# Performance work log

Measured on AMD Instinct MI355X. Metric: run time of the kernel, lower is better.

The kernel has to match this reference:

```python
import jax, jax.numpy as jnp
import numpy as np

B, T, C, H = 8, 2048, 1024, 64


def setup_inputs() -> dict:
    key = jax.random.key(0)
    k1, k2, k3, k4 = jax.random.split(key, 4)
    data = jax.random.normal(k1, (B, T, C), dtype=jnp.float32)
    # nn.Linear(embed, head, bias=False) weights, stored as [embed, head] so y = x @ W
    scale = C ** -0.5  # init-scale so activations stay O(1)
    Wq = jax.random.normal(k2, (C, H), dtype=jnp.float32) * scale
    Wk = jax.random.normal(k3, (C, H), dtype=jnp.float32) * scale
    Wv = jax.random.normal(k4, (C, H), dtype=jnp.float32) * scale
    return {"data": data, "Wq": Wq, "Wk": Wk, "Wv": Wv}


def reference(data, Wq, Wk, Wv):
    # data: [B, T, C]; self-attention (crossData=None), causal mask, eval-mode dropout.
    Bs, Ts, Cs = data.shape
    q = data @ Wq  # [B, T, H]
    k = data @ Wk  # [B, T, H]
    v = data @ Wv  # [B, T, H]
    # NOTE: original scales by C**-0.5 with C = embed_size (faithful to source).
    wei = jnp.einsum('btd,bsd->bts', q, k) * (Cs ** -0.5)  # [B, T, T]
    causal = jnp.tril(jnp.ones((Ts, Ts), dtype=bool))
    wei = jnp.where(causal[None, :, :], wei, -jnp.inf)
    wei = jax.nn.softmax(wei, axis=-1)
    out = jnp.einsum('bts,bsh->bth', wei, v)  # [B, T, H]
    return out
```

## Files before the change

kernel.cpp:

```cpp
#include <hip/hip_runtime.h>
#include <hip/hip_bf16.h>


typedef __bf16 bf16;
typedef __bf16 bf16x8 __attribute__((ext_vector_type(8)));
typedef float f32x4 __attribute__((ext_vector_type(4)));
typedef unsigned int u32;
typedef u32 u32x2 __attribute__((ext_vector_type(2)));
typedef u32 u32x4 __attribute__((ext_vector_type(4)));

#define T_SZ 2048
#define C_SZ 1024
#define H_SZ 64
#define QOFF 0
#define KOFF 1024
#define VOFF 2048
#define PPITCH 72
#define NEG_BIG (-30000.0f)
#define QSCALE 0.04508422f

__device__ __forceinline__ bf16x8 ld8(const bf16* p) { return *(const bf16x8*)p; }

template <int CTRL>
__device__ __forceinline__ float dpp_mov(float x) {
  return __builtin_bit_cast(float,
      __builtin_amdgcn_update_dpp(0, __builtin_bit_cast(int, x), CTRL, 0xf, 0xf, true));
}
__device__ __forceinline__ float qmax16(float x) {
  x = fmaxf(x, dpp_mov<0x121>(x));
  x = fmaxf(x, dpp_mov<0x122>(x));
  x = fmaxf(x, dpp_mov<0x124>(x));
  x = fmaxf(x, dpp_mov<0x128>(x));
  return x;
}
__device__ __forceinline__ float qsum16(float x) {
  x += dpp_mov<0x121>(x);
  x += dpp_mov<0x122>(x);
  x += dpp_mov<0x124>(x);
  x += dpp_mov<0x128>(x);
  return x;
}

__global__ __launch_bounds__(256) void transpose_w(const float* __restrict__ Wq,
                                                   const float* __restrict__ Wk,
                                                   const float* __restrict__ Wv,
                                                   bf16* __restrict__ Wp) {
  __shared__ float sh[64][65];
  int ct = blockIdx.x;
  int mat = blockIdx.y;
  const float* W = (mat == 0) ? Wq : (mat == 1 ? Wk : Wv);
  int tid = threadIdx.x;
  int r = tid >> 2, cb = (tid & 3) * 16;

  const f32x4* src = (const f32x4*)(W + (size_t)(ct * 64 + r) * H_SZ + cb);
#pragma unroll
  for (int v = 0; v < 4; ++v) {
    f32x4 x = src[v];
#pragma unroll
    for (int jx = 0; jx < 4; ++jx) sh[r][cb + v * 4 + jx] = x[jx];
  }
  __syncthreads();

  float scale = (mat == 0) ? QSCALE : 1.0f;
  bf16x8 o0, o1;
#pragma unroll
  for (int jx = 0; jx < 8; ++jx) o0[jx] = (bf16)(sh[cb + jx][r] * scale);
#pragma unroll
  for (int jx = 0; jx < 8; ++jx) o1[jx] = (bf16)(sh[cb + 8 + jx][r] * scale);

  int jj = mat * 4 + (r >> 4);
  int l15 = r & 15;
  int c0 = ct * 64 + cb;
  int kci = c0 >> 5;
  int qa = (c0 >> 3) & 3;
  bf16* dst = Wp + (size_t)(jj * 32 + kci) * 512 + l15 * 32 + qa * 8;
  *(bf16x8*)dst = o0;
  *(bf16x8*)(dst + 8) = o1;
}

__global__ __launch_bounds__(768, 3) void qkv(const float* data, const bf16* __restrict__ Wp,
                                              bf16* arena, int regsz) {
  __shared__ bf16 As[64 * 1024];
  char* As_b = (char*)As;
  int blk = blockIdx.x;
  int tid = threadIdx.x;
  int w = tid >> 6, lane = tid & 63;
  int l15 = lane & 15, quad = lane >> 4;

  const float* src = data + (size_t)blk * 64 * C_SZ;
#pragma unroll
  for (int g = 0; g < 3; ++g) {
    f32x4 st[7];
#pragma unroll
    for (int i = 0; i < 7; ++i) {
      int u = (g * 7 + i) * 768 + tid;
      st[i] = __builtin_nontemporal_load(
          (const f32x4*)(src + (size_t)(u >> 8) * C_SZ + (u & 255) * 4));
    }
#pragma unroll
    for (int i = 0; i < 7; ++i) {
      int u = (g * 7 + i) * 768 + tid;
      int row = u >> 8, c4 = u & 255;
      bf16 t4[4] = {(bf16)st[i][0], (bf16)st[i][1], (bf16)st[i][2], (bf16)st[i][3]};
      int bo = ((c4 >> 3) << 12) + row * 64 + (c4 & 7) * 8;
      *(u32x2*)(As_b + bo) = *(const u32x2*)t4;
    }
  }
  if (tid < 256) {
    int c4 = tid;
    f32x4 x = __builtin_nontemporal_load(
        (const f32x4*)(src + (size_t)63 * C_SZ + c4 * 4));
    bf16 t4[4] = {(bf16)x[0], (bf16)x[1], (bf16)x[2], (bf16)x[3]};
    int bo = ((c4 >> 3) << 12) + 63 * 64 + (c4 & 7) * 8;
    *(u32x2*)(As_b + bo) = *(const u32x2*)t4;
  }
  __syncthreads();

  int j = w;
  const bf16* wb = Wp + (size_t)j * 32 * 512 + l15 * 32 + quad * 8;
  bf16x8 wf[2];
  wf[0] = ld8(wb);
  wf[1] = ld8(wb + 512);

  f32x4 acc[4];
  f32x4 zero = {0.f, 0.f, 0.f, 0.f};
#pragma unroll
  for (int rg = 0; rg < 4; ++rg) acc[rg] = zero;

  bool isQK = (j < 8);
  int lbase = l15 * 64 + quad * 16;

#pragma unroll 2
  for (int kci = 0; kci < 32; ++kci) {
    int cur = kci & 1;
    bf16x8 df[4];
#pragma unroll
    for (int rg = 0; rg < 4; ++rg) {
      int bo = (kci << 12) + rg * 1024 + lbase;
      df[rg] = ld8((const bf16*)(As_b + bo));
    }
    if (isQK) {
#pragma unroll
      for (int rg = 0; rg < 4; ++rg)
        acc[rg] = __builtin_amdgcn_mfma_f32_16x16x32_bf16(wf[cur], df[rg], acc[rg], 0, 0, 0);
    } else {
#pragma unroll
      for (int rg = 0; rg < 4; ++rg)
        acc[rg] = __builtin_amdgcn_mfma_f32_16x16x32_bf16(df[rg], wf[cur], acc[rg], 0, 0, 0);
    }
    wf[cur] = ld8(wb + ((kci + 2) & 31) * 512);
  }

#pragma unroll
  for (int rg = 0; rg < 4; ++rg) {
    bf16* reg = arena + (size_t)(blk * 4 + rg) * (size_t)regsz;
    bf16 p4[4] = {(bf16)acc[rg][0], (bf16)acc[rg][1], (bf16)acc[rg][2], (bf16)acc[rg][3]};
    if (j < 4) {
      bf16* dst = reg + QOFF + l15 * 64 + j * 16 + quad * 4;
      *(u32x2*)dst = *(const u32x2*)p4;
    } else if (j < 8) {
      int jk = j - 4;
      bf16* dst = reg + KOFF + (jk >> 1) * 512 + l15 * 32 + (jk & 1) * 16 + quad * 4;
      *(u32x2*)dst = *(const u32x2*)p4;
    } else {
      bf16* dst = reg + VOFF + ((j - 8) * 16 + l15) * 16 + quad * 4;
      *(u32x2*)dst = *(const u32x2*)p4;
    }
  }
}

__global__ __launch_bounds__(256, 4) void attn(const bf16* __restrict__ arena,
                                               float* __restrict__ out, int regsz) {
  __shared__ bf16 Ps[4][16 * PPITCH];
  __shared__ f32x4 Mg[3][6][64];
  int id = blockIdx.x;
  int b = id & 7;
  int t = id >> 3;
  int slice = t & 3;
  int qt = 31 - (t >> 2);
  int tid = threadIdx.x;
  int w = tid >> 6, lane = tid & 63;
  int l15 = lane & 15, quad = lane >> 4;

  const bf16* base = arena + (size_t)b * 128 * (size_t)regsz;

  const bf16* qreg = base + (size_t)(qt * 4 + slice) * (size_t)regsz + QOFF + l15 * 64;
  bf16x8 qf0 = ld8(qreg + quad * 8);
  bf16x8 qf1 = ld8(qreg + 32 + quad * 8);

  f32x4 accO[4];
  f32x4 zero = {0.f, 0.f, 0.f, 0.f};
#pragma unroll
  for (int nt = 0; nt < 4; ++nt) accO[nt] = zero;
  float m[4], l[4];
#pragma unroll
  for (int r = 0; r < 4; ++r) { m[r] = NEG_BIG; l[r] = 0.f; }

  int qrow_base = qt * 64 + slice * 16 + quad * 4;
  int vro = (quad >> 1);
  int vco = (quad & 1) * 8;

  int q4 = (qt + 4) >> 2;
  int kbeg = w * q4;
  int kend = min((w + 1) * q4, qt + 1);

  for (int kt = kbeg; kt < kend; ++kt) {
    bf16x8 kf[8];
#pragma unroll
    for (int nt = 0; nt < 4; ++nt) {
      const bf16* kp = base + (size_t)(kt * 4 + nt) * (size_t)regsz + KOFF + l15 * 32 + quad * 8;
      kf[2 * nt] = ld8(kp);
      kf[2 * nt + 1] = ld8(kp + 512);
    }

    f32x4 sA[4];
#pragma unroll
    for (int nt = 0; nt < 4; ++nt) sA[nt] = zero;
#pragma unroll
    for (int nt = 0; nt < 4; ++nt) {
      sA[nt] = __builtin_amdgcn_mfma_f32_16x16x32_bf16(qf0, kf[2 * nt], sA[nt], 0, 0, 0);
      sA[nt] = __builtin_amdgcn_mfma_f32_16x16x32_bf16(qf1, kf[2 * nt + 1], sA[nt], 0, 0, 0);
    }

    bf16x8 vf0[4];
#pragma unroll
    for (int nt = 0; nt < 4; ++nt) {
      const bf16* vp = base + (size_t)(kt * 4 + vro) * (size_t)regsz + VOFF +
                       (nt * 16 + l15) * 16 + vco;
      vf0[nt] = ld8(vp);
    }

    if (kt == qt) {
#pragma unroll
      for (int nt = 0; nt < 4; ++nt) {
        int colg = kt * 64 + nt * 16 + l15;
#pragma unroll
        for (int r = 0; r < 4; ++r)
          if (colg > qrow_base + r) sA[nt][r] = NEG_BIG;
      }
    }

    float alpha[4];
#pragma unroll
    for (int r = 0; r < 4; ++r) {
      float mx = qmax16(fmaxf(fmaxf(sA[0][r], sA[1][r]), fmaxf(sA[2][r], sA[3][r])));
      float mnew = fmaxf(m[r], mx);
      alpha[r] = exp2f(m[r] - mnew);
      m[r] = mnew;
    }

    float rs[4] = {0.f, 0.f, 0.f, 0.f};
#pragma unroll
    for (int nt = 0; nt < 4; ++nt) {
#pragma unroll
      for (int r = 0; r < 4; ++r) {
        float p = exp2f(sA[nt][r] - m[r]);
        sA[nt][r] = p;
        rs[r] += p;
      }
    }
#pragma unroll
    for (int r = 0; r < 4; ++r) l[r] = l[r] * alpha[r] + qsum16(rs[r]);

#pragma unroll
    for (int nt = 0; nt < 4; ++nt) {
#pragma unroll
      for (int r = 0; r < 4; ++r)
        Ps[w][(quad * 4 + r) * PPITCH + nt * 16 + l15] = (bf16)sA[nt][r];
    }

    bf16x8 vf1[4];
#pragma unroll
    for (int nt = 0; nt < 4; ++nt) {
      const bf16* vp = base + (size_t)(kt * 4 + 2 + vro) * (size_t)regsz + VOFF +
                       (nt * 16 + l15) * 16 + vco;
      vf1[nt] = ld8(vp);
    }

#pragma unroll
    for (int nt = 0; nt < 4; ++nt) {
#pragma unroll
      for (int r = 0; r < 4; ++r) accO[nt][r] *= alpha[r];
    }
    bf16x8 pf0 = ld8((const bf16*)Ps[w] + l15 * PPITCH + quad * 8);
    bf16x8 pf1 = ld8((const bf16*)Ps[w] + l15 * PPITCH + 32 + quad * 8);
#pragma unroll
    for (int nt = 0; nt < 4; ++nt)
      accO[nt] = __builtin_amdgcn_mfma_f32_16x16x32_bf16(pf0, vf0[nt], accO[nt], 0, 0, 0);
#pragma unroll
    for (int nt = 0; nt < 4; ++nt)
      accO[nt] = __builtin_amdgcn_mfma_f32_16x16x32_bf16(pf1, vf1[nt], accO[nt], 0, 0, 0);
  }

  if (w > 0) {
#pragma unroll
    for (int nt = 0; nt < 4; ++nt) Mg[w - 1][nt][lane] = accO[nt];
    f32x4 mv = {m[0], m[1], m[2], m[3]};
    f32x4 lv = {l[0], l[1], l[2], l[3]};
    Mg[w - 1][4][lane] = mv;
    Mg[w - 1][5][lane] = lv;
  }
  __syncthreads();
  if (w == 0) {
#pragma unroll
    for (int wv = 0; wv < 3; ++wv) {
      f32x4 mo = Mg[wv][4][lane];
      f32x4 lo = Mg[wv][5][lane];
      f32x4 oo[4];
#pragma unroll
      for (int nt = 0; nt < 4; ++nt) oo[nt] = Mg[wv][nt][lane];
#pragma unroll
      for (int r = 0; r < 4; ++r) {
        float mnew = fmaxf(m[r], mo[r]);
        float a = exp2f(m[r] - mnew);
        float bs = exp2f(mo[r] - mnew);
        l[r] = l[r] * a + lo[r] * bs;
#pragma unroll
        for (int nt = 0; nt < 4; ++nt) accO[nt][r] = accO[nt][r] * a + oo[nt][r] * bs;
        m[r] = mnew;
      }
    }

    float inv[4];
#pragma unroll
    for (int r = 0; r < 4; ++r) inv[r] = 1.f / l[r];
#pragma unroll
    for (int nt = 0; nt < 4; ++nt) {
#pragma unroll
      for (int r = 0; r < 4; ++r) {
        int tk = qt * 64 + slice * 16 + quad * 4 + r;
        int h = nt * 16 + l15;
        out[((size_t)b * T_SZ + tk) * H_SZ + h] = accO[nt][r] * inv[r];
      }
    }
  }
}

extern "C" void kernel_launch(void* const* d_in, const int* in_sizes, int n_in,
                              void* d_out, int out_size, void* d_ws, size_t ws_size,
                              hipStream_t stream) {
  const float* data = (const float*)d_in[0];

  const size_t arena_bytes = (size_t)1024 * 4096 * sizeof(bf16);
  const size_t wt_bytes = (size_t)3 * H_SZ * C_SZ * sizeof(bf16);
  bool ws_ok = (d_ws != nullptr) && (ws_size >= arena_bytes + wt_bytes);

  bf16* arena = ws_ok ? (bf16*)d_ws : (bf16*)d_in[0];
  bf16* Wp = ws_ok ? (bf16*)((char*)d_ws + arena_bytes) : (bf16*)d_out;
  int regsz = ws_ok ? 4096 : 32768;

  transpose_w<<<dim3(16, 3), 256, 0, stream>>>((const float*)d_in[1],
                                               (const float*)d_in[2],
                                               (const float*)d_in[3], Wp);
  qkv<<<256, 768, 0, stream>>>(data, Wp, arena, regsz);
  attn<<<1024, 256, 0, stream>>>(arena, (float*)d_out, regsz);
}
```

Before: 130.0 us.

## Double-buffer QKV projection input staging to overlap global loads with MFMA

The qkv kernel used to load and convert the full 64x1024 fp32 input tile into a 128KB LDS buffer before any MFMA work. It now stages the K dimension in four 256-column chunks across two 32KB LDS buffers, issuing global loads for the next chunk before computing on the current one. This is meant to hide global load latency behind matrix math and to cut LDS use, which could raise occupancy. The cost is a block-wide barrier per chunk and more live registers for the prefetched data.

Measured after the change: 131.6 us. Within noise of the previous version (+1.2%).

```diff
diff --git a/kernel.cpp b/kernel.cpp
--- a/kernel.cpp
+++ b/kernel.cpp
@@ -80,7 +80,7 @@
 
 __global__ __launch_bounds__(768, 3) void qkv(const float* data, const bf16* __restrict__ Wp,
                                               bf16* arena, int regsz) {
-  __shared__ bf16 As[64 * 1024];
+  __shared__ bf16 As[2 * 16384];
   char* As_b = (char*)As;
   int blk = blockIdx.x;
   int tid = threadIdx.x;
@@ -88,31 +88,26 @@
   int l15 = lane & 15, quad = lane >> 4;
 
   const float* src = data + (size_t)blk * 64 * C_SZ;
-#pragma unroll
-  for (int g = 0; g < 3; ++g) {
-    f32x4 st[7];
-#pragma unroll
-    for (int i = 0; i < 7; ++i) {
-      int u = (g * 7 + i) * 768 + tid;
+
+  f32x4 st[6];
+#pragma unroll
+  for (int i = 0; i < 6; ++i) {
+    if (i < 5 || tid < 256) {
+      int v = i * 768 + tid;
+      int row = v >> 6, c4l = v & 63;
       st[i] = __builtin_nontemporal_load(
-          (const f32x4*)(src + (size_t)(u >> 8) * C_SZ + (u & 255) * 4));
-    }
-#pragma unroll
-    for (int i = 0; i < 7; ++i) {
-      int u = (g * 7 + i) * 768 + tid;
-      int row = u >> 8, c4 = u & 255;
+          (const f32x4*)(src + (size_t)row * C_SZ + c4l * 4));
+    }
+  }
+#pragma unroll
+  for (int i = 0; i < 6; ++i) {
+    if (i < 5 || tid < 256) {
+      int v = i * 768 + tid;
+      int row = v >> 6, c4l = v & 63;
       bf16 t4[4] = {(bf16)st[i][0], (bf16)st[i][1], (bf16)st[i][2], (bf16)st[i][3]};
-      int bo = ((c4 >> 3) << 12) + row * 64 + (c4 & 7) * 8;
+      int bo = ((c4l >> 3) << 12) + row * 64 + (c4l & 7) * 8;
       *(u32x2*)(As_b + bo) = *(const u32x2*)t4;
     }
-  }
-  if (tid < 256) {
-    int c4 = tid;
-    f32x4 x = __builtin_nontemporal_load(
-        (const f32x4*)(src + (size_t)63 * C_SZ + c4 * 4));
-    bf16 t4[4] = {(bf16)x[0], (bf16)x[1], (bf16)x[2], (bf16)x[3]};
-    int bo = ((c4 >> 3) << 12) + 63 * 64 + (c4 & 7) * 8;
-    *(u32x2*)(As_b + bo) = *(const u32x2*)t4;
   }
   __syncthreads();
 
@@ -130,25 +125,56 @@
   bool isQK = (j < 8);
   int lbase = l15 * 64 + quad * 16;
 
-#pragma unroll 2
-  for (int kci = 0; kci < 32; ++kci) {
-    int cur = kci & 1;
-    bf16x8 df[4];
-#pragma unroll
-    for (int rg = 0; rg < 4; ++rg) {
-      int bo = (kci << 12) + rg * 1024 + lbase;
-      df[rg] = ld8((const bf16*)(As_b + bo));
-    }
-    if (isQK) {
+#pragma unroll
+  for (int c = 0; c < 4; ++c) {
+    if (c < 3) {
+#pragma unroll
+      for (int i = 0; i < 6; ++i) {
+        if (i < 5 || tid < 256) {
+          int v = i * 768 + tid;
+          int row = v >> 6, c4l = v & 63;
+          st[i] = __builtin_nontemporal_load(
+              (const f32x4*)(src + (size_t)row * C_SZ + ((c + 1) * 64 + c4l) * 4));
+        }
+      }
+      __builtin_amdgcn_sched_barrier(0);
+    }
+
+    int rb = (c & 1) * 32768;
+#pragma unroll
+    for (int kl = 0; kl < 8; ++kl) {
+      int kci = c * 8 + kl;
+      int cur = kci & 1;
+      bf16x8 df[4];
 #pragma unroll
       for (int rg = 0; rg < 4; ++rg)
-        acc[rg] = __builtin_amdgcn_mfma_f32_16x16x32_bf16(wf[cur], df[rg], acc[rg], 0, 0, 0);
-    } else {
-#pragma unroll
-      for (int rg = 0; rg < 4; ++rg)
-        acc[rg] = __builtin_amdgcn_mfma_f32_16x16x32_bf16(df[rg], wf[cur], acc[rg], 0, 0, 0);
-    }
-    wf[cur] = ld8(wb + ((kci + 2) & 31) * 512);
+        df[rg] = ld8((const bf16*)(As_b + rb + (kl << 12) + rg * 1024 + lbase));
+      if (isQK) {
+#pragma unroll
+        for (int rg = 0; rg < 4; ++rg)
+          acc[rg] = __builtin_amdgcn_mfma_f32_16x16x32_bf16(wf[cur], df[rg], acc[rg], 0, 0, 0);
+      } else {
+#pragma unroll
+        for (int rg = 0; rg < 4; ++rg)
+          acc[rg] = __builtin_amdgcn_mfma_f32_16x16x32_bf16(df[rg], wf[cur], acc[rg], 0, 0, 0);
+      }
+      wf[cur] = ld8(wb + ((kci + 2) & 31) * 512);
+    }
+
+    if (c < 3) {
+      int wbuf = ((c + 1) & 1) * 32768;
+#pragma unroll
+      for (int i = 0; i < 6; ++i) {
+        if (i < 5 || tid < 256) {
+          int v = i * 768 + tid;
+          int row = v >> 6, c4l = v & 63;
+          bf16 t4[4] = {(bf16)st[i][0], (bf16)st[i][1], (bf16)st[i][2], (bf16)st[i][3]};
+          int bo = wbuf + ((c4l >> 3) << 12) + row * 64 + (c4l & 7) * 8;
+          *(u32x2*)(As_b + bo) = *(const u32x2*)t4;
+        }
+      }
+    }
+    __syncthreads();
   }
 
 #pragma unroll
```

## Split QKV projection into 32-row blocks with two output tiles per wave

Applied to the files above, without the earlier changes.

The QKV projection kernel now handles 32 rows per block instead of 64, using 384 threads and launching 512 blocks instead of 256. Each wave computes two 16-column weight tiles over two row groups, instead of one weight tile over four row groups. The goal is more blocks, filling more of the GPU's compute units, and a smaller LDS footprint for better occupancy. In exchange, each weight fragment is reused across fewer rows, so weights are loaded from global memory twice as often in total.

Result: slower. 134.9 us (+3.8%).

```diff
diff --git a/kernel.cpp b/kernel.cpp
--- a/kernel.cpp
+++ b/kernel.cpp
@@ -78,93 +78,106 @@
   *(bf16x8*)(dst + 8) = o1;
 }
 
-__global__ __launch_bounds__(768, 3) void qkv(const float* data, const bf16* __restrict__ Wp,
+__global__ __launch_bounds__(384, 3) void qkv(const float* data, const bf16* __restrict__ Wp,
                                               bf16* arena, int regsz) {
-  __shared__ bf16 As[64 * 1024];
+  __shared__ bf16 As[32 * 1024];
   char* As_b = (char*)As;
   int blk = blockIdx.x;
   int tid = threadIdx.x;
   int w = tid >> 6, lane = tid & 63;
   int l15 = lane & 15, quad = lane >> 4;
 
-  const float* src = data + (size_t)blk * 64 * C_SZ;
+  const float* src = data + (size_t)blk * 32 * C_SZ;
 #pragma unroll
   for (int g = 0; g < 3; ++g) {
     f32x4 st[7];
 #pragma unroll
     for (int i = 0; i < 7; ++i) {
-      int u = (g * 7 + i) * 768 + tid;
+      int u = (g * 7 + i) * 384 + tid;
       st[i] = __builtin_nontemporal_load(
           (const f32x4*)(src + (size_t)(u >> 8) * C_SZ + (u & 255) * 4));
     }
 #pragma unroll
     for (int i = 0; i < 7; ++i) {
-      int u = (g * 7 + i) * 768 + tid;
+      int u = (g * 7 + i) * 384 + tid;
       int row = u >> 8, c4 = u & 255;
       bf16 t4[4] = {(bf16)st[i][0], (bf16)st[i][1], (bf16)st[i][2], (bf16)st[i][3]};
-      int bo = ((c4 >> 3) << 12) + row * 64 + (c4 & 7) * 8;
+      int bo = ((c4 >> 3) << 11) + row * 64 + (c4 & 7) * 8;
       *(u32x2*)(As_b + bo) = *(const u32x2*)t4;
     }
   }
-  if (tid < 256) {
-    int c4 = tid;
+  if (tid < 128) {
+    int u = 8064 + tid;
+    int row = u >> 8, c4 = u & 255;
     f32x4 x = __builtin_nontemporal_load(
-        (const f32x4*)(src + (size_t)63 * C_SZ + c4 * 4));
+        (const f32x4*)(src + (size_t)row * C_SZ + c4 * 4));
     bf16 t4[4] = {(bf16)x[0], (bf16)x[1], (bf16)x[2], (bf16)x[3]};
-    int bo = ((c4 >> 3) << 12) + 63 * 64 + (c4 & 7) * 8;
+    int bo = ((c4 >> 3) << 11) + row * 64 + (c4 & 7) * 8;
     *(u32x2*)(As_b + bo) = *(const u32x2*)t4;
   }
   __syncthreads();
 
-  int j = w;
-  const bf16* wb = Wp + (size_t)j * 32 * 512 + l15 * 32 + quad * 8;
-  bf16x8 wf[2];
-  wf[0] = ld8(wb);
-  wf[1] = ld8(wb + 512);
-
-  f32x4 acc[4];
+  int j0 = 2 * w;
+  const bf16* wb0 = Wp + (size_t)j0 * 32 * 512 + l15 * 32 + quad * 8;
+  const bf16* wb1 = wb0 + 32 * 512;
+  bf16x8 wf0[2], wf1[2];
+  wf0[0] = ld8(wb0);
+  wf0[1] = ld8(wb0 + 512);
+  wf1[0] = ld8(wb1);
+  wf1[1] = ld8(wb1 + 512);
+
+  f32x4 acc[2][2];
   f32x4 zero = {0.f, 0.f, 0.f, 0.f};
 #pragma unroll
-  for (int rg = 0; rg < 4; ++rg) acc[rg] = zero;
-
-  bool isQK = (j < 8);
+  for (int jc = 0; jc < 2; ++jc)
+#pragma unroll
+    for (int rg = 0; rg < 2; ++rg) acc[jc][rg] = zero;
+
+  bool isQK = (j0 < 8);
   int lbase = l15 * 64 + quad * 16;
 
 #pragma unroll 2
   for (int kci = 0; kci < 32; ++kci) {
     int cur = kci & 1;
-    bf16x8 df[4];
-#pragma unroll
-    for (int rg = 0; rg < 4; ++rg) {
-      int bo = (kci << 12) + rg * 1024 + lbase;
-      df[rg] = ld8((const bf16*)(As_b + bo));
-    }
+    bf16x8 df[2];
+#pragma unroll
+    for (int rg = 0; rg < 2; ++rg)
+      df[rg] = ld8((const bf16*)(As_b + (kci << 11) + rg * 1024 + lbase));
     if (isQK) {
-#pragma unroll
-      for (int rg = 0; rg < 4; ++rg)
-        acc[rg] = __builtin_amdgcn_mfma_f32_16x16x32_bf16(wf[cur], df[rg], acc[rg], 0, 0, 0);
+      acc[0][0] = __builtin_amdgcn_mfma_f32_16x16x32_bf16(wf0[cur], df[0], acc[0][0], 0, 0, 0);
+      acc[0][1] = __builtin_amdgcn_mfma_f32_16x16x32_bf16(wf0[cur], df[1], acc[0][1], 0, 0, 0);
+      acc[1][0] = __builtin_amdgcn_mfma_f32_16x16x32_bf16(wf1[cur], df[0], acc[1][0], 0, 0, 0);
+      acc[1][1] = __builtin_amdgcn_mfma_f32_16x16x32_bf16(wf1[cur], df[1], acc[1][1], 0, 0, 0);
     } else {
-#pragma unroll
-      for (int rg = 0; rg < 4; ++rg)
-        acc[rg] = __builtin_amdgcn_mfma_f32_16x16x32_bf16(df[rg], wf[cur], acc[rg], 0, 0, 0);
-    }
-    wf[cur] = ld8(wb + ((kci + 2) & 31) * 512);
-  }
-
-#pragma unroll
-  for (int rg = 0; rg < 4; ++rg) {
-    bf16* reg = arena + (size_t)(blk * 4 + rg) * (size_t)regsz;
-    bf16 p4[4] = {(bf16)acc[rg][0], (bf16)acc[rg][1], (bf16)acc[rg][2], (bf16)acc[rg][3]};
-    if (j < 4) {
-      bf16* dst = reg + QOFF + l15 * 64 + j * 16 + quad * 4;
-      *(u32x2*)dst = *(const u32x2*)p4;
-    } else if (j < 8) {
-      int jk = j - 4;
-      bf16* dst = reg + KOFF + (jk >> 1) * 512 + l15 * 32 + (jk & 1) * 16 + quad * 4;
-      *(u32x2*)dst = *(const u32x2*)p4;
-    } else {
-      bf16* dst = reg + VOFF + ((j - 8) * 16 + l15) * 16 + quad * 4;
-      *(u32x2*)dst = *(const u32x2*)p4;
+      acc[0][0] = __builtin_amdgcn_mfma_f32_16x16x32_bf16(df[0], wf0[cur], acc[0][0], 0, 0, 0);
+      acc[0][1] = __builtin_amdgcn_mfma_f32_16x16x32_bf16(df[1], wf0[cur], acc[0][1], 0, 0, 0);
+      acc[1][0] = __builtin_amdgcn_mfma_f32_16x16x32_bf16(df[0], wf1[cur], acc[1][0], 0, 0, 0);
+      acc[1][1] = __builtin_amdgcn_mfma_f32_16x16x32_bf16(df[1], wf1[cur], acc[1][1], 0, 0, 0);
+    }
+    int knx = ((kci + 2) & 31) * 512;
+    wf0[cur] = ld8(wb0 + knx);
+    wf1[cur] = ld8(wb1 + knx);
+  }
+
+#pragma unroll
+  for (int jc = 0; jc < 2; ++jc) {
+    int j = j0 + jc;
+#pragma unroll
+    for (int rg = 0; rg < 2; ++rg) {
+      bf16* reg = arena + (size_t)(blk * 2 + rg) * (size_t)regsz;
+      bf16 p4[4] = {(bf16)acc[jc][rg][0], (bf16)acc[jc][rg][1],
+                    (bf16)acc[jc][rg][2], (bf16)acc[jc][rg][3]};
+      if (j < 4) {
+        bf16* dst = reg + QOFF + l15 * 64 + j * 16 + quad * 4;
+        *(u32x2*)dst = *(const u32x2*)p4;
+      } else if (j < 8) {
+        int jk = j - 4;
+        bf16* dst = reg + KOFF + (jk >> 1) * 512 + l15 * 32 + (jk & 1) * 16 + quad * 4;
+        *(u32x2*)dst = *(const u32x2*)p4;
+      } else {
+        bf16* dst = reg + VOFF + ((j - 8) * 16 + l15) * 16 + quad * 4;
+        *(u32x2*)dst = *(const u32x2*)p4;
+      }
     }
   }
 }
@@ -352,6 +365,6 @@
   transpose_w<<<dim3(16, 3), 256, 0, stream>>>((const float*)d_in[1],
                                                (const float*)d_in[2],
                                                (const float*)d_in[3], Wp);
-  qkv<<<256, 768, 0, stream>>>(data, Wp, arena, regsz);
+  qkv<<<512, 384, 0, stream>>>(data, Wp, arena, regsz);
   attn<<<1024, 256, 0, stream>>>(arena, (float*)d_out, regsz);
 }
```

## Process two 16-row query slices per block and prefetch next K tile

Applied to the files above, without the earlier changes.

Each attention block now handles two 16-row query slices (32 rows) instead of one. The same K and V fragments serve both slices, which halves global K/V loads per query row, and the grid drops from 1024 to 512 blocks. The next K tile is loaded into registers before the current softmax work, and block order now pairs long and short causal rows. In exchange, register pressure roughly doubles (launch bounds lowered from 4 to 2 blocks per CU), occupancy and latency hiding drop, and the shared P buffer is reused serially for both slices.

New measurement: 132.4 us. No clear change (+1.9%).

```diff
diff --git a/kernel.cpp b/kernel.cpp
--- a/kernel.cpp
+++ b/kernel.cpp
@@ -169,34 +169,35 @@
   }
 }
 
-__global__ __launch_bounds__(256, 4) void attn(const bf16* __restrict__ arena,
+__global__ __launch_bounds__(256, 2) void attn(const bf16* __restrict__ arena,
                                                float* __restrict__ out, int regsz) {
   __shared__ bf16 Ps[4][16 * PPITCH];
-  __shared__ f32x4 Mg[3][6][64];
+  __shared__ f32x4 Mg[3][12][64];
   int id = blockIdx.x;
   int b = id & 7;
-  int t = id >> 3;
-  int slice = t & 3;
-  int qt = 31 - (t >> 2);
+  int u = id >> 3;
+  int sp = u & 1;
+  int qt = (u < 32) ? (31 - (u >> 1)) : ((u - 32) >> 1);
   int tid = threadIdx.x;
   int w = tid >> 6, lane = tid & 63;
   int l15 = lane & 15, quad = lane >> 4;
 
   const bf16* base = arena + (size_t)b * 128 * (size_t)regsz;
 
-  const bf16* qreg = base + (size_t)(qt * 4 + slice) * (size_t)regsz + QOFF + l15 * 64;
-  bf16x8 qf0 = ld8(qreg + quad * 8);
-  bf16x8 qf1 = ld8(qreg + 32 + quad * 8);
-
-  f32x4 accO[4];
+  const bf16* qregA = base + (size_t)(qt * 4 + sp * 2) * (size_t)regsz + QOFF + l15 * 64;
+  const bf16* qregB = qregA + regsz;
+  bf16x8 qfA0 = ld8(qregA + quad * 8), qfA1 = ld8(qregA + 32 + quad * 8);
+  bf16x8 qfB0 = ld8(qregB + quad * 8), qfB1 = ld8(qregB + 32 + quad * 8);
+
+  f32x4 accA[4], accB[4];
   f32x4 zero = {0.f, 0.f, 0.f, 0.f};
 #pragma unroll
-  for (int nt = 0; nt < 4; ++nt) accO[nt] = zero;
-  float m[4], l[4];
-#pragma unroll
-  for (int r = 0; r < 4; ++r) { m[r] = NEG_BIG; l[r] = 0.f; }
-
-  int qrow_base = qt * 64 + slice * 16 + quad * 4;
+  for (int nt = 0; nt < 4; ++nt) { accA[nt] = zero; accB[nt] = zero; }
+  float mA[4], lA[4], mB[4], lB[4];
+#pragma unroll
+  for (int r = 0; r < 4; ++r) { mA[r] = NEG_BIG; lA[r] = 0.f; mB[r] = NEG_BIG; lB[r] = 0.f; }
+
+  int rowA = qt * 64 + sp * 32 + quad * 4;
   int vro = (quad >> 1);
   int vco = (quad & 1) * 8;
 
@@ -204,24 +205,15 @@
   int kbeg = w * q4;
   int kend = min((w + 1) * q4, qt + 1);
 
+  bf16x8 kf[8];
+#pragma unroll
+  for (int nt = 0; nt < 4; ++nt) {
+    const bf16* kp = base + (size_t)(kbeg * 4 + nt) * (size_t)regsz + KOFF + l15 * 32 + quad * 8;
+    kf[2 * nt] = ld8(kp);
+    kf[2 * nt + 1] = ld8(kp + 512);
+  }
+
   for (int kt = kbeg; kt < kend; ++kt) {
-    bf16x8 kf[8];
-#pragma unroll
-    for (int nt = 0; nt < 4; ++nt) {
-      const bf16* kp = base + (size_t)(kt * 4 + nt) * (size_t)regsz + KOFF + l15 * 32 + quad * 8;
-      kf[2 * nt] = ld8(kp);
-      kf[2 * nt + 1] = ld8(kp + 512);
-    }
-
-    f32x4 sA[4];
-#pragma unroll
-    for (int nt = 0; nt < 4; ++nt) sA[nt] = zero;
-#pragma unroll
-    for (int nt = 0; nt < 4; ++nt) {
-      sA[nt] = __builtin_amdgcn_mfma_f32_16x16x32_bf16(qf0, kf[2 * nt], sA[nt], 0, 0, 0);
-      sA[nt] = __builtin_amdgcn_mfma_f32_16x16x32_bf16(qf1, kf[2 * nt + 1], sA[nt], 0, 0, 0);
-    }
-
     bf16x8 vf0[4];
 #pragma unroll
     for (int nt = 0; nt < 4; ++nt) {
@@ -230,43 +222,28 @@
       vf0[nt] = ld8(vp);
     }
 
-    if (kt == qt) {
+    f32x4 sA[4], sB[4];
+#pragma unroll
+    for (int nt = 0; nt < 4; ++nt) { sA[nt] = zero; sB[nt] = zero; }
+#pragma unroll
+    for (int nt = 0; nt < 4; ++nt) {
+      sA[nt] = __builtin_amdgcn_mfma_f32_16x16x32_bf16(qfA0, kf[2 * nt], sA[nt], 0, 0, 0);
+      sA[nt] = __builtin_amdgcn_mfma_f32_16x16x32_bf16(qfA1, kf[2 * nt + 1], sA[nt], 0, 0, 0);
+    }
+#pragma unroll
+    for (int nt = 0; nt < 4; ++nt) {
+      sB[nt] = __builtin_amdgcn_mfma_f32_16x16x32_bf16(qfB0, kf[2 * nt], sB[nt], 0, 0, 0);
+      sB[nt] = __builtin_amdgcn_mfma_f32_16x16x32_bf16(qfB1, kf[2 * nt + 1], sB[nt], 0, 0, 0);
+    }
+
+    if (kt + 1 < kend) {
 #pragma unroll
       for (int nt = 0; nt < 4; ++nt) {
-        int colg = kt * 64 + nt * 16 + l15;
-#pragma unroll
-        for (int r = 0; r < 4; ++r)
-          if (colg > qrow_base + r) sA[nt][r] = NEG_BIG;
-      }
-    }
-
-    float alpha[4];
-#pragma unroll
-    for (int r = 0; r < 4; ++r) {
-      float mx = qmax16(fmaxf(fmaxf(sA[0][r], sA[1][r]), fmaxf(sA[2][r], sA[3][r])));
-      float mnew = fmaxf(m[r], mx);
-      alpha[r] = exp2f(m[r] - mnew);
-      m[r] = mnew;
-    }
-
-    float rs[4] = {0.f, 0.f, 0.f, 0.f};
-#pragma unroll
-    for (int nt = 0; nt < 4; ++nt) {
-#pragma unroll
-      for (int r = 0; r < 4; ++r) {
-        float p = exp2f(sA[nt][r] - m[r]);
-        sA[nt][r] = p;
-        rs[r] += p;
-      }
-    }
-#pragma unroll
-    for (int r = 0; r < 4; ++r) l[r] = l[r] * alpha[r] + qsum16(rs[r]);
-
-#pragma unroll
-    for (int nt = 0; nt < 4; ++nt) {
-#pragma unroll
-      for (int r = 0; r < 4; ++r)
-        Ps[w][(quad * 4 + r) * PPITCH + nt * 16 + l15] = (bf16)sA[nt][r];
+        const bf16* kp = base + (size_t)((kt + 1) * 4 + nt) * (size_t)regsz + KOFF +
+                         l15 * 32 + quad * 8;
+        kf[2 * nt] = ld8(kp);
+        kf[2 * nt + 1] = ld8(kp + 512);
+      }
     }
 
     bf16x8 vf1[4];
@@ -277,60 +254,150 @@
       vf1[nt] = ld8(vp);
     }
 
-#pragma unroll
-    for (int nt = 0; nt < 4; ++nt) {
-#pragma unroll
-      for (int r = 0; r < 4; ++r) accO[nt][r] *= alpha[r];
-    }
-    bf16x8 pf0 = ld8((const bf16*)Ps[w] + l15 * PPITCH + quad * 8);
-    bf16x8 pf1 = ld8((const bf16*)Ps[w] + l15 * PPITCH + 32 + quad * 8);
+    if (kt == qt) {
+#pragma unroll
+      for (int nt = 0; nt < 4; ++nt) {
+        int colg = kt * 64 + nt * 16 + l15;
+#pragma unroll
+        for (int r = 0; r < 4; ++r) {
+          if (colg > rowA + r) sA[nt][r] = NEG_BIG;
+          if (colg > rowA + 16 + r) sB[nt][r] = NEG_BIG;
+        }
+      }
+    }
+
+    float alA[4], alB[4];
+#pragma unroll
+    for (int r = 0; r < 4; ++r) {
+      float mx = qmax16(fmaxf(fmaxf(sA[0][r], sA[1][r]), fmaxf(sA[2][r], sA[3][r])));
+      float mnew = fmaxf(mA[r], mx);
+      alA[r] = exp2f(mA[r] - mnew);
+      mA[r] = mnew;
+    }
+#pragma unroll
+    for (int r = 0; r < 4; ++r) {
+      float mx = qmax16(fmaxf(fmaxf(sB[0][r], sB[1][r]), fmaxf(sB[2][r], sB[3][r])));
+      float mnew = fmaxf(mB[r], mx);
+      alB[r] = exp2f(mB[r] - mnew);
+      mB[r] = mnew;
+    }
+
+    float rsA[4] = {0.f, 0.f, 0.f, 0.f}, rsB[4] = {0.f, 0.f, 0.f, 0.f};
+#pragma unroll
+    for (int nt = 0; nt < 4; ++nt) {
+#pragma unroll
+      for (int r = 0; r < 4; ++r) {
+        float pA = exp2f(sA[nt][r] - mA[r]);
+        sA[nt][r] = pA;
+        rsA[r] += pA;
+        float pB = exp2f(sB[nt][r] - mB[r]);
+        sB[nt][r] = pB;
+        rsB[r] += pB;
+      }
+    }
+#pragma unroll
+    for (int r = 0; r < 4; ++r) {
+      lA[r] = lA[r] * alA[r] + qsum16(rsA[r]);
+      lB[r] = lB[r] * alB[r] + qsum16(rsB[r]);
+    }
+
 #pragma unroll
     for (int nt = 0; nt < 4; ++nt)
-      accO[nt] = __builtin_amdgcn_mfma_f32_16x16x32_bf16(pf0, vf0[nt], accO[nt], 0, 0, 0);
+#pragma unroll
+      for (int r = 0; r < 4; ++r)
+        Ps[w][(quad * 4 + r) * PPITCH + nt * 16 + l15] = (bf16)sA[nt][r];
 #pragma unroll
     for (int nt = 0; nt < 4; ++nt)
-      accO[nt] = __builtin_amdgcn_mfma_f32_16x16x32_bf16(pf1, vf1[nt], accO[nt], 0, 0, 0);
+#pragma unroll
+      for (int r = 0; r < 4; ++r) accA[nt][r] *= alA[r];
+    {
+      bf16x8 pf0 = ld8((const bf16*)Ps[w] + l15 * PPITCH + quad * 8);
+      bf16x8 pf1 = ld8((const bf16*)Ps[w] + l15 * PPITCH + 32 + quad * 8);
+#pragma unroll
+      for (int nt = 0; nt < 4; ++nt)
+        accA[nt] = __builtin_amdgcn_mfma_f32_16x16x32_bf16(pf0, vf0[nt], accA[nt], 0, 0, 0);
+#pragma unroll
+      for (int nt = 0; nt < 4; ++nt)
+        accA[nt] = __builtin_amdgcn_mfma_f32_16x16x32_bf16(pf1, vf1[nt], accA[nt], 0, 0, 0);
+    }
+
+#pragma unroll
+    for (int nt = 0; nt < 4; ++nt)
+#pragma unroll
+      for (int r = 0; r < 4; ++r)
+        Ps[w][(quad * 4 + r) * PPITCH + nt * 16 + l15] = (bf16)sB[nt][r];
+#pragma unroll
+    for (int nt = 0; nt < 4; ++nt)
+#pragma unroll
+      for (int r = 0; r < 4; ++r) accB[nt][r] *= alB[r];
+    {
+      bf16x8 pf0 = ld8((const bf16*)Ps[w] + l15 * PPITCH + quad * 8);
+      bf16x8 pf1 = ld8((const bf16*)Ps[w] + l15 * PPITCH + 32 + quad * 8);
+#pragma unroll
+      for (int nt = 0; nt < 4; ++nt)
+        accB[nt] = __builtin_amdgcn_mfma_f32_16x16x32_bf16(pf0, vf0[nt], accB[nt], 0, 0, 0);
+#pragma unroll
+      for (int nt = 0; nt < 4; ++nt)
+        accB[nt] = __builtin_amdgcn_mfma_f32_16x16x32_bf16(pf1, vf1[nt], accB[nt], 0, 0, 0);
+    }
   }
 
   if (w > 0) {
 #pragma unroll
-    for (int nt = 0; nt < 4; ++nt) Mg[w - 1][nt][lane] = accO[nt];
-    f32x4 mv = {m[0], m[1], m[2], m[3]};
-    f32x4 lv = {l[0], l[1], l[2], l[3]};
-    Mg[w - 1][4][lane] = mv;
-    Mg[w - 1][5][lane] = lv;
+    for (int nt = 0; nt < 4; ++nt) {
+      Mg[w - 1][nt][lane] = accA[nt];
+      Mg[w - 1][4 + nt][lane] = accB[nt];
+    }
+    f32x4 v8 = {mA[0], mA[1], mA[2], mA[3]};
+    f32x4 v9 = {lA[0], lA[1], lA[2], lA[3]};
+    f32x4 v10 = {mB[0], mB[1], mB[2], mB[3]};
+    f32x4 v11 = {lB[0], lB[1], lB[2], lB[3]};
+    Mg[w - 1][8][lane] = v8;
+    Mg[w - 1][9][lane] = v9;
+    Mg[w - 1][10][lane] = v10;
+    Mg[w - 1][11][lane] = v11;
   }
   __syncthreads();
   if (w == 0) {
 #pragma unroll
     for (int wv = 0; wv < 3; ++wv) {
-      f32x4 mo = Mg[wv][4][lane];
-      f32x4 lo = Mg[wv][5][lane];
-      f32x4 oo[4];
-#pragma unroll
-      for (int nt = 0; nt < 4; ++nt) oo[nt] = Mg[wv][nt][lane];
+      f32x4 moA = Mg[wv][8][lane], loA = Mg[wv][9][lane];
+      f32x4 moB = Mg[wv][10][lane], loB = Mg[wv][11][lane];
 #pragma unroll
       for (int r = 0; r < 4; ++r) {
-        float mnew = fmaxf(m[r], mo[r]);
-        float a = exp2f(m[r] - mnew);
-        float bs = exp2f(mo[r] - mnew);
-        l[r] = l[r] * a + lo[r] * bs;
-#pragma unroll
-        for (int nt = 0; nt < 4; ++nt) accO[nt][r] = accO[nt][r] * a + oo[nt][r] * bs;
-        m[r] = mnew;
-      }
-    }
-
-    float inv[4];
-#pragma unroll
-    for (int r = 0; r < 4; ++r) inv[r] = 1.f / l[r];
-#pragma unroll
-    for (int nt = 0; nt < 4; ++nt) {
+        float mnew = fmaxf(mA[r], moA[r]);
+        float a = exp2f(mA[r] - mnew);
+        float bs = exp2f(moA[r] - mnew);
+        lA[r] = lA[r] * a + loA[r] * bs;
+#pragma unroll
+        for (int nt = 0; nt < 4; ++nt)
+          accA[nt][r] = accA[nt][r] * a + Mg[wv][nt][lane][r] * bs;
+        mA[r] = mnew;
+      }
 #pragma unroll
       for (int r = 0; r < 4; ++r) {
-        int tk = qt * 64 + slice * 16 + quad * 4 + r;
+        float mnew = fmaxf(mB[r], moB[r]);
+        float a = exp2f(mB[r] - mnew);
+        float bs = exp2f(moB[r] - mnew);
+        lB[r] = lB[r] * a + loB[r] * bs;
+#pragma unroll
+        for (int nt = 0; nt < 4; ++nt)
+          accB[nt][r] = accB[nt][r] * a + Mg[wv][4 + nt][lane][r] * bs;
+        mB[r] = mnew;
+      }
+    }
+
+    float invA[4], invB[4];
+#pragma unroll
+    for (int r = 0; r < 4; ++r) { invA[r] = 1.f / lA[r]; invB[r] = 1.f / lB[r]; }
+#pragma unroll
+    for (int nt = 0; nt < 4; ++nt) {
+#pragma unroll
+      for (int r = 0; r < 4; ++r) {
+        int tA = qt * 64 + sp * 32 + quad * 4 + r;
         int h = nt * 16 + l15;
-        out[((size_t)b * T_SZ + tk) * H_SZ + h] = accO[nt][r] * inv[r];
+        out[((size_t)b * T_SZ + tA) * H_SZ + h] = accA[nt][r] * invA[r];
+        out[((size_t)b * T_SZ + tA + 16) * H_SZ + h] = accB[nt][r] * invB[r];
       }
     }
   }
@@ -353,5 +420,5 @@
                                                (const float*)d_in[2],
                                                (const float*)d_in[3], Wp);
   qkv<<<256, 768, 0, stream>>>(data, Wp, arena, regsz);
-  attn<<<1024, 256, 0, stream>>>(arena, (float*)d_out, regsz);
-}
+  attn<<<512, 256, 0, stream>>>(arena, (float*)d_out, regsz);
+}
```
